# Optimization experiments

Measured on AMD Instinct MI355X. Metric: run time of the kernel, lower is better.

Reference implementation:

```python
import jax, jax.numpy as jnp
import numpy as np

GH, GW = 16, 16          # group_size
DIM = 512
H = 8                    # num_heads
PD = DIM // 16           # pos_dim = (dim//4)//4 = 32
B = 256                  # number of groups (batch*windows)
N = GH * GW


def _make_bias_tables():
    # biases buffer: all 2D relative offsets, shape [(2GH-1)*(2GW-1), 2]
    h = np.arange(1 - GH, GH)
    w = np.arange(1 - GW, GW)
    bh, bw = np.meshgrid(h, w, indexing='ij')
    biases = np.stack([bh, bw]).reshape(2, -1).T.astype(np.float32)
    # relative_position_index: [N, N] lookup into the bias table
    ch, cw = np.meshgrid(np.arange(GH), np.arange(GW), indexing='ij')
    coords = np.stack([ch, cw]).reshape(2, -1)            # [2, N]
    rel = coords[:, :, None] - coords[:, None, :]         # [2, N, N]
    rel = rel.transpose(1, 2, 0).copy()                   # [N, N, 2]
    rel[:, :, 0] += GH - 1
    rel[:, :, 1] += GW - 1
    rel[:, :, 0] *= 2 * GW - 1
    idx = rel.sum(-1)
    return biases, idx.astype(np.int32)


def _ln(x, g, b, eps=1e-5):
    m = x.mean(-1, keepdims=True)
    v = ((x - m) ** 2).mean(-1, keepdims=True)
    return (x - m) / jnp.sqrt(v + eps) * g + b


def setup_inputs() -> dict:
    key = jax.random.key(0)
    ks = jax.random.split(key, 16)
    s = 0.02
    biases_np, idx_np = _make_bias_tables()
    return {
        'x': jax.random.normal(ks[0], (B, N, DIM), dtype=jnp.float32),
        'qkv_w': jax.random.normal(ks[1], (DIM, 3 * DIM), dtype=jnp.float32) * s,
        'qkv_b': jnp.zeros((3 * DIM,), jnp.float32),
        'proj_w': jax.random.normal(ks[2], (DIM, DIM), dtype=jnp.float32) * s,
        'proj_b': jnp.zeros((DIM,), jnp.float32),
        'p1_w': jax.random.normal(ks[3], (2, PD), dtype=jnp.float32) * s,
        'p1_b': jnp.zeros((PD,), jnp.float32),
        'g1': jnp.ones((PD,), jnp.float32), 'b1': jnp.zeros((PD,), jnp.float32),
        'p2_w': jax.random.normal(ks[4], (PD, PD), dtype=jnp.float32) * s,
        'p2_b': jnp.zeros((PD,), jnp.float32),
        'g2': jnp.ones((PD,), jnp.float32), 'b2': jnp.zeros((PD,), jnp.float32),
        'p3_w': jax.random.normal(ks[5], (PD, PD), dtype=jnp.float32) * s,
        'p3_b': jnp.zeros((PD,), jnp.float32),
        'g3': jnp.ones((PD,), jnp.float32), 'b3': jnp.zeros((PD,), jnp.float32),
        'p4_w': jax.random.normal(ks[6], (PD, H), dtype=jnp.float32) * s,
        'p4_b': jnp.zeros((H,), jnp.float32),
        'biases': jnp.asarray(biases_np),
        'rel_idx': jnp.asarray(idx_np),
    }


def reference(x, qkv_w, qkv_b, proj_w, proj_b,
              p1_w, p1_b, g1, b1, p2_w, p2_b, g2, b2,
              p3_w, p3_b, g3, b3, p4_w, p4_b, biases, rel_idx):
    Bn, Nn, C = x.shape
    hd = C // H
    scale = hd ** -0.5
    qkv = (x @ qkv_w + qkv_b).reshape(Bn, Nn, 3, H, hd).transpose(2, 0, 3, 1, 4)
    q, k, v = qkv[0] * scale, qkv[1], qkv[2]      # [B, H, N, hd]
    attn = jnp.einsum('bhnd,bhmd->bhnm', q, k)    # [B, H, N, N]
    # dynamic position bias MLP on the offset table
    h1 = jax.nn.relu(_ln(biases @ p1_w + p1_b, g1, b1))
    h2 = jax.nn.relu(_ln(h1 @ p2_w + p2_b, g2, b2))
    h3 = jax.nn.relu(_ln(h2 @ p3_w + p3_b, g3, b3))
    pos = h3 @ p4_w + p4_b                        # [L, H]
    rpb = pos[rel_idx.reshape(-1)].reshape(Nn, Nn, H).transpose(2, 0, 1)  # [H, N, N]
    attn = jax.nn.softmax(attn + rpb[None], axis=-1)
    out = jnp.einsum('bhnm,bhmd->bhnd', attn, v)
    out = out.transpose(0, 2, 1, 3).reshape(Bn, Nn, C)
    return out @ proj_w + proj_b
```

## Files before the change

### kernel.cpp

```cpp
#include <hip/hip_runtime.h>
#include <stdint.h>

typedef __bf16 bf16x8 __attribute__((ext_vector_type(8)));
typedef float  f32x4  __attribute__((ext_vector_type(4)));
typedef unsigned short ushort_t;

#define MFMA16(a,b,c) __builtin_amdgcn_mfma_f32_16x16x32_bf16((a),(b),(c),0,0,0)

#define GLOAD16(gsrc, ldst) \
    __builtin_amdgcn_global_load_lds((const __attribute__((address_space(1))) void*)(gsrc), \
                                     (__attribute__((address_space(3))) void*)(ldst), 16, 0, 0)

#define BATCH 256
#define NTOK  256
#define DIM   512
#define NH    8
#define HD    64
#define PD    32
#define LTAB  961
#define MROWS (BATCH*NTOK)

#define POS_OFF   0
#define RPB_OFF   32768
#define WQKV_OFF  (RPB_OFF + 2097152)
#define WPROJ_OFF (WQKV_OFF + 1572864)
#define QKV_OFF   (WPROJ_OFF + 524288)
#define AOUT_OFF  (QKV_OFF + 201326592)
#define XB_OFF    AOUT_OFF

__device__ __forceinline__ ushort_t f2bf(float f) {
    unsigned int u = __builtin_bit_cast(unsigned int, f);
    u += 0x7FFFu + ((u >> 16) & 1u);
    return (ushort_t)(u >> 16);
}

__global__ __launch_bounds__(256) void convert_x(
    const float* __restrict__ x, ushort_t* __restrict__ xb)
{
    size_t i = ((size_t)blockIdx.x * 256 + threadIdx.x) * 8;
    float4 f0 = *(const float4*)(x + i);
    float4 f1 = *(const float4*)(x + i + 4);
    uint4 o;
    o.x = (unsigned)f2bf(f0.x) | ((unsigned)f2bf(f0.y) << 16);
    o.y = (unsigned)f2bf(f0.z) | ((unsigned)f2bf(f0.w) << 16);
    o.z = (unsigned)f2bf(f1.x) | ((unsigned)f2bf(f1.y) << 16);
    o.w = (unsigned)f2bf(f1.z) | ((unsigned)f2bf(f1.w) << 16);
    *reinterpret_cast<uint4*>(xb + i) = o;
}

__global__ __launch_bounds__(256) void convert_w(
    const float* __restrict__ qkv_w, const float* __restrict__ proj_w,
    ushort_t* __restrict__ wqkvT, ushort_t* __restrict__ wprojT)
{
    int i = blockIdx.x * 256 + threadIdx.x;
    int n = i >> 9, k = i & 511;
    wqkvT[i] = f2bf(qkv_w[(size_t)k * 1536 + n]);
    if (i < 512 * 512) {
        int n2 = i >> 9, k2 = i & 511;
        wprojT[i] = f2bf(proj_w[(size_t)k2 * 512 + n2]);
    }
}

__device__ __forceinline__ float ln_relu_t(float h, int j,
                                           const float* __restrict__ g,
                                           const float* __restrict__ bb) {
    float m = h;
    m += __shfl_xor(m, 1); m += __shfl_xor(m, 2); m += __shfl_xor(m, 4);
    m += __shfl_xor(m, 8); m += __shfl_xor(m, 16);
    m *= (1.0f / PD);
    float d = h - m;
    float v = d * d;
    v += __shfl_xor(v, 1); v += __shfl_xor(v, 2); v += __shfl_xor(v, 4);
    v += __shfl_xor(v, 8); v += __shfl_xor(v, 16);
    v *= (1.0f / PD);
    float x = d * rsqrtf(v + 1e-5f) * g[j] + bb[j];
    return x > 0.f ? x : 0.f;
}

__global__ __launch_bounds__(256) void pos_mlp(
    const float* __restrict__ biases,
    const float* __restrict__ p1_w, const float* __restrict__ p1_b,
    const float* __restrict__ g1, const float* __restrict__ b1,
    const float* __restrict__ p2_w, const float* __restrict__ p2_b,
    const float* __restrict__ g2, const float* __restrict__ b2,
    const float* __restrict__ p3_w, const float* __restrict__ p3_b,
    const float* __restrict__ g3, const float* __restrict__ b3,
    const float* __restrict__ p4_w, const float* __restrict__ p4_b,
    float* __restrict__ pos)
{
    __shared__ float hs[8][33];
    int tid = threadIdx.x;
    int rl = tid >> 5, j = tid & 31;
    int r = blockIdx.x * 8 + rl;
    bool ok = r < LTAB;
    float c0 = ok ? biases[r * 2 + 0] : 0.f;
    float c1 = ok ? biases[r * 2 + 1] : 0.f;

    float h = c0 * p1_w[j] + c1 * p1_w[PD + j] + p1_b[j];
    h = ln_relu_t(h, j, g1, b1);

    hs[rl][j] = h;
    __syncthreads();
    float s = p2_b[j];
#pragma unroll
    for (int i = 0; i < PD; i++) s += hs[rl][i] * p2_w[i * PD + j];
    __syncthreads();
    h = ln_relu_t(s, j, g2, b2);

    hs[rl][j] = h;
    __syncthreads();
    s = p3_b[j];
#pragma unroll
    for (int i = 0; i < PD; i++) s += hs[rl][i] * p3_w[i * PD + j];
    __syncthreads();
    h = ln_relu_t(s, j, g3, b3);

    hs[rl][j] = h;
    __syncthreads();
    if (ok && j < NH) {
        float o = p4_b[j];
#pragma unroll
        for (int i = 0; i < PD; i++) o += hs[rl][i] * p4_w[i * NH + j];
        pos[r * NH + j] = o;
    }
}

__global__ __launch_bounds__(256) void rpb_gather(
    const float* __restrict__ pos, const int* __restrict__ rel_idx,
    float* __restrict__ rpb)
{
    int i = blockIdx.x * 256 + threadIdx.x;
    int idx = rel_idx[i];
#pragma unroll
    for (int hh = 0; hh < NH; hh++) rpb[(size_t)hh * 65536 + i] = pos[idx * NH + hh];
}

__global__ __launch_bounds__(256) void qkv_gemm(
    const ushort_t* __restrict__ xb, const ushort_t* __restrict__ wT,
    const float* __restrict__ qkv_b, ushort_t* __restrict__ qkvb)
{
    __shared__ ushort_t As[128 * 32];
    __shared__ ushort_t Bs[128 * 32];
    int t = threadIdx.x;
    int bid = blockIdx.x;
    int mt = bid / 12, nt = bid % 12;
    int m0 = mt * 128, n0 = nt * 128;
    int lane = t & 63, w = t >> 6;
    int wm = w >> 1, wn = w & 1;
    int lr = lane & 15, lk = lane >> 4;
    int srow = lane >> 2, scol = (lane & 3) * 8;
    f32x4 acc[4][4];
#pragma unroll
    for (int fr = 0; fr < 4; fr++)
#pragma unroll
        for (int fc = 0; fc < 4; fc++) acc[fr][fc] = (f32x4){0.f, 0.f, 0.f, 0.f};

    for (int kt = 0; kt < 16; ++kt) {
        __syncthreads();
#pragma unroll
        for (int i = 0; i < 2; i++) {
            int row = w * 32 + i * 16;
            GLOAD16(xb + (size_t)(m0 + row + srow) * 512 + kt * 32 + scol,
                    As + (row) * 32);
            GLOAD16(wT + (size_t)(n0 + row + srow) * 512 + kt * 32 + scol,
                    Bs + (row) * 32);
        }
        asm volatile("s_waitcnt vmcnt(0)" ::: "memory");
        __syncthreads();
        bf16x8 a[4], b[4];
#pragma unroll
        for (int fr = 0; fr < 4; fr++)
            a[fr] = *reinterpret_cast<const bf16x8*>(&As[(wm * 64 + fr * 16 + lr) * 32 + lk * 8]);
#pragma unroll
        for (int fc = 0; fc < 4; fc++)
            b[fc] = *reinterpret_cast<const bf16x8*>(&Bs[(wn * 64 + fc * 16 + lr) * 32 + lk * 8]);
#pragma unroll
        for (int fr = 0; fr < 4; fr++)
#pragma unroll
            for (int fc = 0; fc < 4; fc++)
                acc[fr][fc] = MFMA16(a[fr], b[fc], acc[fr][fc]);
    }
    int s = n0 >> 9;
    if (s < 2) {
        float sc = (s == 0) ? 0.125f : 1.0f;
#pragma unroll
        for (int fc = 0; fc < 4; fc++) {
            int n = n0 + wn * 64 + fc * 16 + lr;
            float bias = qkv_b[n];
            int hh = (n >> 6) & 7, d = n & 63;
#pragma unroll
            for (int fr = 0; fr < 4; fr++)
#pragma unroll
                for (int r = 0; r < 4; r++) {
                    int m = m0 + wm * 64 + fr * 16 + lk * 4 + r;
                    int bg = m >> 8, tok = m & 255;
                    float v = (acc[fr][fc][r] + bias) * sc;
                    qkvb[((((size_t)s * 256 + bg) * 8 + hh) * 256 + tok) * 64 + d] = f2bf(v);
                }
        }
    } else {
#pragma unroll
        for (int fc = 0; fc < 4; fc++) {
            int n = n0 + wn * 64 + fc * 16 + lr;
            float bias = qkv_b[n];
            int hh = (n >> 6) & 7, d = n & 63;
#pragma unroll
            for (int fr = 0; fr < 4; fr++) {
                int m = m0 + wm * 64 + fr * 16 + lk * 4;
                int bg = m >> 8, tok = m & 255;
                uint2 pk;
                pk.x = (unsigned)f2bf(acc[fr][fc][0] + bias) |
                       ((unsigned)f2bf(acc[fr][fc][1] + bias) << 16);
                pk.y = (unsigned)f2bf(acc[fr][fc][2] + bias) |
                       ((unsigned)f2bf(acc[fr][fc][3] + bias) << 16);
                *reinterpret_cast<uint2*>(
                    qkvb + ((((size_t)512 + bg) * 8 + hh) * 64 + d) * 256 + tok) = pk;
            }
        }
    }
}

__global__ __launch_bounds__(256) void attn_kernel(
    const ushort_t* __restrict__ qkvb, const float* __restrict__ rpb,
    ushort_t* __restrict__ aout)
{
    __shared__ ushort_t Ps[4][32][40];
    int t = threadIdx.x, lane = t & 63, w = t >> 6;
    int bid = blockIdx.x;
    int qh = bid & 1; int bh = bid >> 1; int hh = bh & 7; int bg = bh >> 3;
    const ushort_t* Qg  = qkvb + (((size_t)bg * 8 + hh) * 256) * 64;
    const ushort_t* Kg  = qkvb + (((size_t)(256 + bg) * 8 + hh) * 256) * 64;
    const ushort_t* VTg = qkvb + (((size_t)(512 + bg) * 8 + hh) * 64) * 256;
    int lr = lane & 15, lk = lane >> 4;
    int qrow0 = qh * 128 + w * 32;

    bf16x8 qf[2][2];
#pragma unroll
    for (int fr = 0; fr < 2; fr++)
#pragma unroll
        for (int kc = 0; kc < 2; kc++)
            qf[fr][kc] = *reinterpret_cast<const bf16x8*>(
                Qg + (size_t)(qrow0 + fr * 16 + lr) * 64 + kc * 32 + lk * 8);

    f32x4 oacc[2][4];
    float rsum[2][4];
#pragma unroll
    for (int fr = 0; fr < 2; fr++) {
#pragma unroll
        for (int fc = 0; fc < 4; fc++) oacc[fr][fc] = (f32x4){0.f, 0.f, 0.f, 0.f};
#pragma unroll
        for (int r = 0; r < 4; r++) rsum[fr][r] = 0.f;
    }

    for (int kt = 0; kt < 8; ++kt) {
        f32x4 sacc[2][2];
#pragma unroll
        for (int fr = 0; fr < 2; fr++)
#pragma unroll
            for (int fc = 0; fc < 2; fc++) sacc[fr][fc] = (f32x4){0.f, 0.f, 0.f, 0.f};
#pragma unroll
        for (int kc = 0; kc < 2; kc++) {
            bf16x8 kb0 = *reinterpret_cast<const bf16x8*>(
                Kg + (size_t)(kt * 32 + lr) * 64 + kc * 32 + lk * 8);
            bf16x8 kb1 = *reinterpret_cast<const bf16x8*>(
                Kg + (size_t)(kt * 32 + 16 + lr) * 64 + kc * 32 + lk * 8);
            sacc[0][0] = MFMA16(qf[0][kc], kb0, sacc[0][0]);
            sacc[0][1] = MFMA16(qf[0][kc], kb1, sacc[0][1]);
            sacc[1][0] = MFMA16(qf[1][kc], kb0, sacc[1][0]);
            sacc[1][1] = MFMA16(qf[1][kc], kb1, sacc[1][1]);
        }
#pragma unroll
        for (int fr = 0; fr < 2; fr++)
#pragma unroll
            for (int fc = 0; fc < 2; fc++)
#pragma unroll
                for (int r = 0; r < 4; r++) {
                    int row = qrow0 + fr * 16 + lk * 4 + r;
                    int col = kt * 32 + fc * 16 + lr;
                    float lg = sacc[fr][fc][r] + rpb[((size_t)hh * 256 + row) * 256 + col];
                    float p = __expf(lg);
                    rsum[fr][r] += p;
                    Ps[w][fr * 16 + lk * 4 + r][fc * 16 + lr] = f2bf(p);
                }
        bf16x8 pa[2], vb[4];
#pragma unroll
        for (int fr = 0; fr < 2; fr++)
            pa[fr] = *reinterpret_cast<const bf16x8*>(&Ps[w][fr * 16 + lr][lk * 8]);
#pragma unroll
        for (int fc = 0; fc < 4; fc++)
            vb[fc] = *reinterpret_cast<const bf16x8*>(
                VTg + (size_t)(fc * 16 + lr) * 256 + kt * 32 + lk * 8);
#pragma unroll
        for (int fr = 0; fr < 2; fr++)
#pragma unroll
            for (int fc = 0; fc < 4; fc++)
                oacc[fr][fc] = MFMA16(pa[fr], vb[fc], oacc[fr][fc]);
    }
#pragma unroll
    for (int fr = 0; fr < 2; fr++)
#pragma unroll
        for (int r = 0; r < 4; r++) {
            float s = rsum[fr][r];
            s += __shfl_xor(s, 1); s += __shfl_xor(s, 2);
            s += __shfl_xor(s, 4); s += __shfl_xor(s, 8);
            rsum[fr][r] = s;
        }
#pragma unroll
    for (int fr = 0; fr < 2; fr++)
#pragma unroll
        for (int fc = 0; fc < 4; fc++)
#pragma unroll
            for (int r = 0; r < 4; r++) {
                int tok = qrow0 + fr * 16 + lk * 4 + r;
                int d = fc * 16 + lr;
                float ov = oacc[fr][fc][r] / rsum[fr][r];
                aout[((size_t)bg * 256 + tok) * 512 + hh * 64 + d] = f2bf(ov);
            }
}

__global__ __launch_bounds__(256) void proj_gemm(
    const ushort_t* __restrict__ ain, const ushort_t* __restrict__ wT,
    const float* __restrict__ proj_b, float* __restrict__ out)
{
    __shared__ ushort_t As[128 * 32];
    __shared__ ushort_t Bs[128 * 32];
    int t = threadIdx.x;
    int bid = blockIdx.x;
    int mt = bid / 4, nt = bid % 4;
    int m0 = mt * 128, n0 = nt * 128;
    int lane = t & 63, w = t >> 6;
    int wm = w >> 1, wn = w & 1;
    int lr = lane & 15, lk = lane >> 4;
    int srow = lane >> 2, scol = (lane & 3) * 8;
    f32x4 acc[4][4];
#pragma unroll
    for (int fr = 0; fr < 4; fr++)
#pragma unroll
        for (int fc = 0; fc < 4; fc++) acc[fr][fc] = (f32x4){0.f, 0.f, 0.f, 0.f};

    for (int kt = 0; kt < 16; ++kt) {
        __syncthreads();
#pragma unroll
        for (int i = 0; i < 2; i++) {
            int row = w * 32 + i * 16;
            GLOAD16(ain + (size_t)(m0 + row + srow) * 512 + kt * 32 + scol,
                    As + (row) * 32);
            GLOAD16(wT + (size_t)(n0 + row + srow) * 512 + kt * 32 + scol,
                    Bs + (row) * 32);
        }
        asm volatile("s_waitcnt vmcnt(0)" ::: "memory");
        __syncthreads();
        bf16x8 a[4], b[4];
#pragma unroll
        for (int fr = 0; fr < 4; fr++)
            a[fr] = *reinterpret_cast<const bf16x8*>(&As[(wm * 64 + fr * 16 + lr) * 32 + lk * 8]);
#pragma unroll
        for (int fc = 0; fc < 4; fc++)
            b[fc] = *reinterpret_cast<const bf16x8*>(&Bs[(wn * 64 + fc * 16 + lr) * 32 + lk * 8]);
#pragma unroll
        for (int fr = 0; fr < 4; fr++)
#pragma unroll
            for (int fc = 0; fc < 4; fc++)
                acc[fr][fc] = MFMA16(a[fr], b[fc], acc[fr][fc]);
    }
#pragma unroll
    for (int fc = 0; fc < 4; fc++) {
        int n = n0 + wn * 64 + fc * 16 + lr;
        float bias = proj_b[n];
#pragma unroll
        for (int fr = 0; fr < 4; fr++)
#pragma unroll
            for (int r = 0; r < 4; r++) {
                int m = m0 + wm * 64 + fr * 16 + lk * 4 + r;
                out[(size_t)m * 512 + n] = acc[fr][fc][r] + bias;
            }
    }
}

extern "C" void kernel_launch(void* const* d_in, const int* in_sizes, int n_in,
                              void* d_out, int out_size, void* d_ws, size_t ws_size,
                              hipStream_t stream) {
    const float* x      = (const float*)d_in[0];
    const float* qkv_w  = (const float*)d_in[1];
    const float* qkv_b  = (const float*)d_in[2];
    const float* proj_w = (const float*)d_in[3];
    const float* proj_b = (const float*)d_in[4];
    const float* p1_w = (const float*)d_in[5];
    const float* p1_b = (const float*)d_in[6];
    const float* g1   = (const float*)d_in[7];
    const float* b1   = (const float*)d_in[8];
    const float* p2_w = (const float*)d_in[9];
    const float* p2_b = (const float*)d_in[10];
    const float* g2   = (const float*)d_in[11];
    const float* b2   = (const float*)d_in[12];
    const float* p3_w = (const float*)d_in[13];
    const float* p3_b = (const float*)d_in[14];
    const float* g3   = (const float*)d_in[15];
    const float* b3   = (const float*)d_in[16];
    const float* p4_w = (const float*)d_in[17];
    const float* p4_b = (const float*)d_in[18];
    const float* biases  = (const float*)d_in[19];
    const int*   rel_idx = (const int*)d_in[20];
    float* out = (float*)d_out;

    char* ws = (char*)d_ws;
    float*    pos    = (float*)(ws + POS_OFF);
    float*    rpb    = (float*)(ws + RPB_OFF);
    ushort_t* wqkvT  = (ushort_t*)(ws + WQKV_OFF);
    ushort_t* wprojT = (ushort_t*)(ws + WPROJ_OFF);
    ushort_t* qkvb   = (ushort_t*)(ws + QKV_OFF);
    ushort_t* aoutb  = (ushort_t*)(ws + AOUT_OFF);
    ushort_t* xb     = (ushort_t*)(ws + XB_OFF);

    convert_x<<<dim3(16384), dim3(256), 0, stream>>>(x, xb);
    convert_w<<<dim3(3072), dim3(256), 0, stream>>>(qkv_w, proj_w, wqkvT, wprojT);
    pos_mlp<<<dim3(121), dim3(256), 0, stream>>>(biases, p1_w, p1_b, g1, b1,
                                                 p2_w, p2_b, g2, b2,
                                                 p3_w, p3_b, g3, b3,
                                                 p4_w, p4_b, pos);
    rpb_gather<<<dim3(256), dim3(256), 0, stream>>>(pos, rel_idx, rpb);
    qkv_gemm<<<dim3(512 * 12), dim3(256), 0, stream>>>(xb, wqkvT, qkv_b, qkvb);
    attn_kernel<<<dim3(4096), dim3(256), 0, stream>>>(qkvb, rpb, aoutb);
    proj_gemm<<<dim3(512 * 4), dim3(256), 0, stream>>>(aoutb, wprojT, proj_b, out);
}
```

Before: 440.6 us.

## Double-buffer GEMM LDS loads, remap blocks across XCDs, stage attention output stores

Both the QKV and projection GEMMs now use double-buffered LDS. The next K-tile's global-to-LDS load is issued before computing on the current tile, so load latency overlaps with MFMA work. Block indices are remapped so that consecutive tiles are spread across the 8 XCDs. The attention epilogue now multiplies by a reciprocal instead of dividing, and writes output through LDS as 16-byte vector stores instead of scattered 2-byte stores. These changes double the GEMM LDS footprint and add LDS use in attention, which may reduce occupancy.

```diff
diff --git a/kernel.cpp b/kernel.cpp
--- a/kernel.cpp
+++ b/kernel.cpp
@@ -18,7 +18,6 @@
 #define HD    64
 #define PD    32
 #define LTAB  961
-#define MROWS (BATCH*NTOK)
 
 #define POS_OFF   0
 #define RPB_OFF   32768
@@ -139,47 +138,60 @@
     const ushort_t* __restrict__ xb, const ushort_t* __restrict__ wT,
     const float* __restrict__ qkv_b, ushort_t* __restrict__ qkvb)
 {
-    __shared__ ushort_t As[128 * 32];
-    __shared__ ushort_t Bs[128 * 32];
+    __shared__ ushort_t As[2][4096];
+    __shared__ ushort_t Bs[2][4096];
     int t = threadIdx.x;
     int bid = blockIdx.x;
-    int mt = bid / 12, nt = bid % 12;
+    int wgid = (bid & 7) * 768 + (bid >> 3);
+    int mt = wgid / 12, nt = wgid % 12;
     int m0 = mt * 128, n0 = nt * 128;
     int lane = t & 63, w = t >> 6;
     int wm = w >> 1, wn = w & 1;
     int lr = lane & 15, lk = lane >> 4;
     int srow = lane >> 2, scol = (lane & 3) * 8;
+    const ushort_t* Asrc = xb + (size_t)(m0 + srow) * 512 + scol;
+    const ushort_t* Bsrc = wT + (size_t)(n0 + srow) * 512 + scol;
+
     f32x4 acc[4][4];
 #pragma unroll
     for (int fr = 0; fr < 4; fr++)
 #pragma unroll
         for (int fc = 0; fc < 4; fc++) acc[fr][fc] = (f32x4){0.f, 0.f, 0.f, 0.f};
 
+#define QSTAGE(buf, kt) do { \
+    _Pragma("unroll") \
+    for (int i_ = 0; i_ < 2; i_++) { \
+        int row_ = w * 32 + i_ * 16; \
+        GLOAD16(Asrc + (size_t)row_ * 512 + (kt) * 32, &As[buf][row_ * 32]); \
+        GLOAD16(Bsrc + (size_t)row_ * 512 + (kt) * 32, &Bs[buf][row_ * 32]); \
+    } } while (0)
+
+    QSTAGE(0, 0);
+    asm volatile("s_waitcnt vmcnt(0)" ::: "memory");
+    __syncthreads();
+    int cur = 0;
     for (int kt = 0; kt < 16; ++kt) {
-        __syncthreads();
-#pragma unroll
-        for (int i = 0; i < 2; i++) {
-            int row = w * 32 + i * 16;
-            GLOAD16(xb + (size_t)(m0 + row + srow) * 512 + kt * 32 + scol,
-                    As + (row) * 32);
-            GLOAD16(wT + (size_t)(n0 + row + srow) * 512 + kt * 32 + scol,
-                    Bs + (row) * 32);
-        }
-        asm volatile("s_waitcnt vmcnt(0)" ::: "memory");
-        __syncthreads();
+        if (kt < 15) QSTAGE(cur ^ 1, kt + 1);
         bf16x8 a[4], b[4];
 #pragma unroll
         for (int fr = 0; fr < 4; fr++)
-            a[fr] = *reinterpret_cast<const bf16x8*>(&As[(wm * 64 + fr * 16 + lr) * 32 + lk * 8]);
+            a[fr] = *reinterpret_cast<const bf16x8*>(&As[cur][(wm * 64 + fr * 16 + lr) * 32 + lk * 8]);
 #pragma unroll
         for (int fc = 0; fc < 4; fc++)
-            b[fc] = *reinterpret_cast<const bf16x8*>(&Bs[(wn * 64 + fc * 16 + lr) * 32 + lk * 8]);
+            b[fc] = *reinterpret_cast<const bf16x8*>(&Bs[cur][(wn * 64 + fc * 16 + lr) * 32 + lk * 8]);
 #pragma unroll
         for (int fr = 0; fr < 4; fr++)
 #pragma unroll
             for (int fc = 0; fc < 4; fc++)
                 acc[fr][fc] = MFMA16(a[fr], b[fc], acc[fr][fc]);
-    }
+        if (kt < 15) {
+            asm volatile("s_waitcnt vmcnt(0)" ::: "memory");
+            __syncthreads();
+        }
+        cur ^= 1;
+    }
+#undef QSTAGE
+
     int s = n0 >> 9;
     if (s < 2) {
         float sc = (s == 0) ? 0.125f : 1.0f;
@@ -225,6 +237,7 @@
     ushort_t* __restrict__ aout)
 {
     __shared__ ushort_t Ps[4][32][40];
+    __shared__ ushort_t Os[4][16 * 72];
     int t = threadIdx.x, lane = t & 63, w = t >> 6;
     int bid = blockIdx.x;
     int qh = bid & 1; int bh = bid >> 1; int hh = bh & 7; int bg = bh >> 3;
@@ -296,6 +309,7 @@
             for (int fc = 0; fc < 4; fc++)
                 oacc[fr][fc] = MFMA16(pa[fr], vb[fc], oacc[fr][fc]);
     }
+    float rinv[2][4];
 #pragma unroll
     for (int fr = 0; fr < 2; fr++)
 #pragma unroll
@@ -303,66 +317,82 @@
             float s = rsum[fr][r];
             s += __shfl_xor(s, 1); s += __shfl_xor(s, 2);
             s += __shfl_xor(s, 4); s += __shfl_xor(s, 8);
-            rsum[fr][r] = s;
-        }
-#pragma unroll
-    for (int fr = 0; fr < 2; fr++)
+            rinv[fr][r] = __frcp_rn(s);
+        }
+#pragma unroll
+    for (int fr = 0; fr < 2; fr++) {
 #pragma unroll
         for (int fc = 0; fc < 4; fc++)
 #pragma unroll
-            for (int r = 0; r < 4; r++) {
-                int tok = qrow0 + fr * 16 + lk * 4 + r;
-                int d = fc * 16 + lr;
-                float ov = oacc[fr][fc][r] / rsum[fr][r];
-                aout[((size_t)bg * 256 + tok) * 512 + hh * 64 + d] = f2bf(ov);
-            }
+            for (int r = 0; r < 4; r++)
+                Os[w][(lk * 4 + r) * 72 + fc * 16 + lr] = f2bf(oacc[fr][fc][r] * rinv[fr][r]);
+#pragma unroll
+        for (int ii = 0; ii < 2; ii++) {
+            int j = lane + ii * 64;
+            int row = j >> 3, ch = j & 7;
+            uint4 v = *reinterpret_cast<const uint4*>(&Os[w][row * 72 + ch * 8]);
+            *reinterpret_cast<uint4*>(
+                aout + ((size_t)(bg * 256 + qrow0 + fr * 16 + row)) * 512 + hh * 64 + ch * 8) = v;
+        }
+    }
 }
 
 __global__ __launch_bounds__(256) void proj_gemm(
     const ushort_t* __restrict__ ain, const ushort_t* __restrict__ wT,
     const float* __restrict__ proj_b, float* __restrict__ out)
 {
-    __shared__ ushort_t As[128 * 32];
-    __shared__ ushort_t Bs[128 * 32];
+    __shared__ ushort_t As[2][4096];
+    __shared__ ushort_t Bs[2][4096];
     int t = threadIdx.x;
     int bid = blockIdx.x;
-    int mt = bid / 4, nt = bid % 4;
+    int wgid = (bid & 7) * 256 + (bid >> 3);
+    int mt = wgid / 4, nt = wgid % 4;
     int m0 = mt * 128, n0 = nt * 128;
     int lane = t & 63, w = t >> 6;
     int wm = w >> 1, wn = w & 1;
     int lr = lane & 15, lk = lane >> 4;
     int srow = lane >> 2, scol = (lane & 3) * 8;
+    const ushort_t* Asrc = ain + (size_t)(m0 + srow) * 512 + scol;
+    const ushort_t* Bsrc = wT + (size_t)(n0 + srow) * 512 + scol;
     f32x4 acc[4][4];
 #pragma unroll
     for (int fr = 0; fr < 4; fr++)
 #pragma unroll
         for (int fc = 0; fc < 4; fc++) acc[fr][fc] = (f32x4){0.f, 0.f, 0.f, 0.f};
 
+#define PSTAGE(buf, kt) do { \
+    _Pragma("unroll") \
+    for (int i_ = 0; i_ < 2; i_++) { \
+        int row_ = w * 32 + i_ * 16; \
+        GLOAD16(Asrc + (size_t)row_ * 512 + (kt) * 32, &As[buf][row_ * 32]); \
+        GLOAD16(Bsrc + (size_t)row_ * 512 + (kt) * 32, &Bs[buf][row_ * 32]); \
+    } } while (0)
+
+    PSTAGE(0, 0);
+    asm volatile("s_waitcnt vmcnt(0)" ::: "memory");
+    __syncthreads();
+    int cur = 0;
     for (int kt = 0; kt < 16; ++kt) {
-        __syncthreads();
-#pragma unroll
-        for (int i = 0; i < 2; i++) {
-            int row = w * 32 + i * 16;
-            GLOAD16(ain + (size_t)(m0 + row + srow) * 512 + kt * 32 + scol,
-                    As + (row) * 32);
-            GLOAD16(wT + (size_t)(n0 + row + srow) * 512 + kt * 32 + scol,
-                    Bs + (row) * 32);
-        }
-        asm volatile("s_waitcnt vmcnt(0)" ::: "memory");
-        __syncthreads();
+        if (kt < 15) PSTAGE(cur ^ 1, kt + 1);
         bf16x8 a[4], b[4];
 #pragma unroll
         for (int fr = 0; fr < 4; fr++)
-            a[fr] = *reinterpret_cast<const bf16x8*>(&As[(wm * 64 + fr * 16 + lr) * 32 + lk * 8]);
+            a[fr] = *reinterpret_cast<const bf16x8*>(&As[cur][(wm * 64 + fr * 16 + lr) * 32 + lk * 8]);
 #pragma unroll
         for (int fc = 0; fc < 4; fc++)
-            b[fc] = *reinterpret_cast<const bf16x8*>(&Bs[(wn * 64 + fc * 16 + lr) * 32 + lk * 8]);
+            b[fc] = *reinterpret_cast<const bf16x8*>(&Bs[cur][(wn * 64 + fc * 16 + lr) * 32 + lk * 8]);
 #pragma unroll
         for (int fr = 0; fr < 4; fr++)
 #pragma unroll
             for (int fc = 0; fc < 4; fc++)
                 acc[fr][fc] = MFMA16(a[fr], b[fc], acc[fr][fc]);
-    }
+        if (kt < 15) {
+            asm volatile("s_waitcnt vmcnt(0)" ::: "memory");
+            __syncthreads();
+        }
+        cur ^= 1;
+    }
+#undef PSTAGE
 #pragma unroll
     for (int fc = 0; fc < 4; fc++) {
         int n = n0 + wn * 64 + fc * 16 + lr;
```

Result: no change. 446.2 us (+1.3%).
